# Performance work log

Hardware: AMD Instinct MI355X
Metric: run time of the kernel (lower is better)

Reference implementation:

```python
import jax, jax.numpy as jnp
import numpy as np

HID, HEADS = 2048, 16
Q_LORA, KV_LORA = 1536, 512
NOPE, ROPE, VD = 128, 64, 128
N_EXP, TOPK, MOE_I, SH_I = 8, 2, 1408, 2816
EPS, RSF = 1e-6, 1.0
ROPE_BASE = 10000.0


def _rms(x, w):
    return x * jax.lax.rsqrt(jnp.mean(jnp.square(x), -1, keepdims=True) + EPS) * w


def _rope(x, pos):
    # neox-style rotary on last dim; x: [T, H, d], pos: [T]
    d = x.shape[-1]
    inv = 1.0 / (ROPE_BASE ** (jnp.arange(0, d, 2, dtype=jnp.float32) / d))
    ang = pos.astype(jnp.float32)[:, None] * inv  # [T, d/2]
    cos, sin = jnp.cos(ang)[:, None, :], jnp.sin(ang)[:, None, :]
    x1, x2 = x[..., : d // 2], x[..., d // 2:]
    return jnp.concatenate([x1 * cos - x2 * sin, x2 * cos + x1 * sin], -1)


def setup_inputs() -> dict:
    key = jax.random.key(0)
    ks = jax.random.split(key, 16)
    T, s, f = 1024, 0.02, jnp.float32
    return {
        'positions': jnp.arange(T, dtype=jnp.int32),
        'hidden_states': jax.random.normal(ks[0], (T, HID), f),
        'residual': jax.random.normal(ks[1], (T, HID), f),
        'w_in_ln': jnp.ones((HID,), f),
        'w_post_ln': jnp.ones((HID,), f),
        'w_q_ln': jnp.ones((Q_LORA,), f),
        'w_kv_ln': jnp.ones((KV_LORA,), f),
        'w_qkv_a': jax.random.normal(ks[2], (HID, Q_LORA + KV_LORA + ROPE), f) * s,
        'w_q_b': jax.random.normal(ks[3], (Q_LORA, HEADS * (NOPE + ROPE)), f) * s,
        'w_kv_b': jax.random.normal(ks[4], (KV_LORA, HEADS * (NOPE + VD)), f) * s,
        'w_o': jax.random.normal(ks[5], (HEADS * VD, HID), f) * s,
        'gate_w': jax.random.normal(ks[6], (HID, N_EXP), f) * s,
        'we_gate': jax.random.normal(ks[7], (N_EXP, HID, MOE_I), f) * s,
        'we_up': jax.random.normal(ks[8], (N_EXP, HID, MOE_I), f) * s,
        'we_down': jax.random.normal(ks[9], (N_EXP, MOE_I, HID), f) * s,
        'ws_gate': jax.random.normal(ks[10], (HID, SH_I), f) * s,
        'ws_up': jax.random.normal(ks[11], (HID, SH_I), f) * s,
        'ws_down': jax.random.normal(ks[12], (SH_I, HID), f) * s,
    }


def reference(positions, hidden_states, residual, w_in_ln, w_post_ln, w_q_ln, w_kv_ln,
              w_qkv_a, w_q_b, w_kv_b, w_o, gate_w, we_gate, we_up, we_down,
              ws_gate, ws_up, ws_down):
    T = hidden_states.shape[0]
    # fused_add_rms_norm: residual <- x + residual; x <- rmsnorm(residual)
    residual = hidden_states + residual
    h = _rms(residual, w_in_ln)
    # fused qkv_a projection and split
    qkv = h @ w_qkv_a  # [T, q_lora + kv_lora + rope]
    q_c = _rms(qkv[:, :Q_LORA], w_q_ln)
    kv_c = _rms(qkv[:, Q_LORA:Q_LORA + KV_LORA], w_kv_ln)
    k_pe = qkv[:, Q_LORA + KV_LORA:][:, None, :]  # [T, 1, rope]
    # MLA up-projections
    q = (q_c @ w_q_b).reshape(T, HEADS, NOPE + ROPE)
    q_nope, q_pe = q[..., :NOPE], q[..., NOPE:]
    kv = (kv_c @ w_kv_b).reshape(T, HEADS, NOPE + VD)
    k_nope, v = kv[..., :NOPE], kv[..., NOPE:]
    q_pe = _rope(q_pe, positions)
    k_pe = _rope(k_pe, positions)
    q = jnp.concatenate([q_nope, q_pe], -1)  # [T, H, nope+rope]
    k = jnp.concatenate([k_nope, jnp.broadcast_to(k_pe, (T, HEADS, ROPE))], -1)
    scores = jnp.einsum('qhd,khd->hqk', q, k) * (NOPE + ROPE) ** -0.5
    causal = jnp.tril(jnp.ones((T, T), bool))
    scores = jnp.where(causal, scores, jnp.finfo(scores.dtype).min)
    p = jax.nn.softmax(scores, -1)
    attn_out = jnp.einsum('hqk,khd->qhd', p, v).reshape(T, HEADS * VD) @ w_o
    # post-attention fused add + norm
    residual = residual + attn_out
    h = _rms(residual, w_post_ln)
    # MoE gate: softmax scores, top-k, renormalized combine weights
    probs = jax.nn.softmax(h @ gate_w, -1)
    tw, ti = jax.lax.top_k(probs, TOPK)
    tw = tw / jnp.sum(tw, -1, keepdims=True)
    comb = jnp.sum(jax.nn.one_hot(ti, N_EXP, dtype=h.dtype) * tw[..., None], 1)  # [T, E]
    # routed experts (dense grouped-GEMM reference, SwiGLU)
    g = jnp.einsum('th,ehi->eti', h, we_gate)
    u = jnp.einsum('th,ehi->eti', h, we_up)
    y = jnp.einsum('eti,eih->eth', jax.nn.silu(g) * u, we_down)
    routed = jnp.einsum('te,eth->th', comb, y) * RSF
    # shared experts
    shared = (jax.nn.silu(h @ ws_gate) * (h @ ws_up)) @ ws_down
    return routed + shared, residual
```

## Files before the change

### kernel.cpp

```cpp
#include <hip/hip_runtime.h>
#include <hip/hip_bf16.h>

typedef unsigned short u16;
typedef __attribute__((ext_vector_type(8))) short bf16x8;
typedef __attribute__((ext_vector_type(4))) float f32x4;
typedef __attribute__((ext_vector_type(8))) unsigned short u16x8;
typedef __attribute__((ext_vector_type(4))) unsigned short u16x4;

#define T_TOK 1024
#define HID 2048
#define HEADS 16
#define Q_LORA 1536
#define KV_LORA 512
#define NOPE 128
#define ROPED 64
#define VD 128
#define N_EXP 8
#define MOE_I 1408
#define SH_I 2816
#define QKV_N 2112
#define QKV_LD 2176
#define QD 192
#define KVD 256
#define EPSF 1e-6f
#define NEG_BIG (-3.4e38f)

__device__ __forceinline__ u16 f2bf(float f) {
  union { float f; unsigned u; } x; x.f = f;
  unsigned r = x.u + 0x7fffu + ((x.u >> 16) & 1u);
  return (u16)(r >> 16);
}
__device__ __forceinline__ float bf2f(u16 h) {
  union { unsigned u; float f; } x; x.u = ((unsigned)h) << 16; return x.f;
}
__device__ __forceinline__ void split2(float f, u16& hi, u16& lo) {
  hi = f2bf(f);
  lo = f2bf(f - bf2f(hi));
}

__device__ __forceinline__ void gload16(const u16* g, const u16* l) {
  __builtin_amdgcn_global_load_lds(
      (const __attribute__((address_space(1))) void*)g,
      (__attribute__((address_space(3))) void*)l, 16, 0, 0);
}

__device__ __forceinline__ void xcd_unswizzle(int& bx, int& by, int& bz) {
  int gx = gridDim.x, gy = gridDim.y;
  int nwg = gx * gy * gridDim.z;
  int flat = blockIdx.x + gx * (blockIdx.y + gy * blockIdx.z);
  int q8 = nwg >> 3, r8 = nwg & 7;
  int xcd = flat & 7, pos = flat >> 3;
  int wg = (xcd < r8 ? xcd * (q8 + 1) : r8 * (q8 + 1) + (xcd - r8) * q8) + pos;
  bx = wg % gx; int tmp = wg / gx;
  by = tmp % gy; bz = tmp / gy;
}

__device__ __forceinline__ float block_sum(float v, float* s) {
  #pragma unroll
  for (int o = 32; o > 0; o >>= 1) v += __shfl_down(v, o, 64);
  int w = threadIdx.x >> 6, lane = threadIdx.x & 63;
  __syncthreads();
  if (lane == 0) s[w] = v;
  __syncthreads();
  float r = s[0];
  for (int i = 1; i < 4; ++i) r += s[i];
  return r;
}
__device__ __forceinline__ float block_max(float v, float* s) {
  #pragma unroll
  for (int o = 32; o > 0; o >>= 1) v = fmaxf(v, __shfl_down(v, o, 64));
  int w = threadIdx.x >> 6, lane = threadIdx.x & 63;
  __syncthreads();
  if (lane == 0) s[w] = v;
  __syncthreads();
  float r = s[0];
  for (int i = 1; i < 4; ++i) r = fmaxf(r, s[i]);
  return r;
}

__global__ __launch_bounds__(256) void gemm_bf16(
    const u16* __restrict__ A, long asz, int lda,
    const u16* __restrict__ B, long bsz, int ldb,
    float* __restrict__ C, u16* __restrict__ Cb, long csz, int ldc,
    const float* __restrict__ Cadd, const u16* __restrict__ CaddB, int ldcadd,
    int K, float alpha, int causal, int mode,
    float* __restrict__ pbuf, int ksplit, int stot, int soff) {
  int bxi, byi, zz;
  xcd_unswizzle(bxi, byi, zz);
  const int bm = byi << 7, bn = bxi << 7;
  const int z = (ksplit > 1) ? (zz / ksplit) : zz;
  const int s = (ksplit > 1) ? (zz % ksplit) : 0;
  A += (long)z * asz; B += (long)z * bsz;
  if (C) C += (long)z * csz;
  if (Cb) Cb += (long)z * csz;
  if (Cadd && !pbuf) Cadd += (long)z * csz;
  if (CaddB) CaddB += (long)z * csz;
  const int tid = threadIdx.x, lane = tid & 63, wid = tid >> 6;

  if (causal && bn >= bm + 128) return;

  __shared__ alignas(16) u16 As[128 * 32];
  __shared__ alignas(16) u16 Bs[128 * 32];

  const int wr = wid >> 1, wc = wid & 1;
  f32x4 acc[4][4];
  #pragma unroll
  for (int m = 0; m < 4; ++m)
    #pragma unroll
    for (int n = 0; n < 4; ++n) acc[m][n] = f32x4{0.f, 0.f, 0.f, 0.f};

  const int srow = (wid << 5) + (lane >> 2);
  const int scol = (lane & 3) << 3;
  const int arow = (wr << 6) + (lane & 15);
  const int brow = (wc << 6) + (lane & 15);
  const int koff = (lane >> 4) << 3;

  const int kseg = K / ksplit;
  const int kbeg = s * kseg, kend = kbeg + kseg;

  for (int k0 = kbeg; k0 < kend; k0 += 32) {
    #pragma unroll
    for (int c = 0; c < 2; ++c) {
      int row = srow + (c << 4);
      gload16(A + (long)(bm + row) * lda + k0 + scol, &As[(wid << 10) + (c << 9)]);
      gload16(B + (long)(bn + row) * ldb + k0 + scol, &Bs[(wid << 10) + (c << 9)]);
    }
    __syncthreads();
    bf16x8 a[4], b[4];
    #pragma unroll
    for (int m = 0; m < 4; ++m) a[m] = *(const bf16x8*)&As[((arow + (m << 4)) << 5) + koff];
    #pragma unroll
    for (int n = 0; n < 4; ++n) b[n] = *(const bf16x8*)&Bs[((brow + (n << 4)) << 5) + koff];
    #pragma unroll
    for (int m = 0; m < 4; ++m)
      #pragma unroll
      for (int n = 0; n < 4; ++n)
        acc[m][n] = __builtin_amdgcn_mfma_f32_16x16x32_bf16(a[m], b[n], acc[m][n], 0, 0, 0);
    __syncthreads();
  }

  const int rbase = bm + (wr << 6) + ((lane >> 4) << 2);
  const int cbase = bn + (wc << 6) + (lane & 15);

  if (pbuf) {
    long pstride = (long)(gridDim.y << 7) * ldc;
    float* pp = pbuf + ((long)z * stot + soff + s) * pstride;
    #pragma unroll
    for (int m = 0; m < 4; ++m)
      #pragma unroll
      for (int j = 0; j < 4; ++j) {
        int r = rbase + (m << 4) + j;
        #pragma unroll
        for (int n = 0; n < 4; ++n) {
          int cc = cbase + (n << 4);
          pp[(long)r * ldc + cc] = acc[m][n][j];
        }
      }
    return;
  }

  #pragma unroll
  for (int m = 0; m < 4; ++m) {
    #pragma unroll
    for (int j = 0; j < 4; ++j) {
      int r = rbase + (m << 4) + j;
      #pragma unroll
      for (int n = 0; n < 4; ++n) {
        int cc = cbase + (n << 4);
        float v = acc[m][n][j] * alpha;
        if (mode == 0) {
          if (Cadd) v += Cadd[(long)r * ldcadd + cc];
          if (causal && cc > r) v = NEG_BIG;
          C[(long)r * ldc + cc] = v;
        } else if (mode == 1) {
          float gg = Cadd[(long)r * ldcadd + cc];
          float sgv = gg / (1.f + expf(-gg));
          Cb[(long)r * ldc + cc] = f2bf(sgv * v);
        } else if (mode == 2) {
          Cb[(long)r * ldc + cc] = f2bf(v);
        } else {
          float gg = bf2f(CaddB[(long)r * ldcadd + cc]);
          float sgv = gg / (1.f + expf(-gg));
          Cb[(long)r * ldc + cc] = f2bf(sgv * v);
        }
      }
    }
  }
}

__global__ __launch_bounds__(256) void reduce_sk(
    const float* __restrict__ pbuf, long pstride, int S,
    float* __restrict__ C, u16* __restrict__ Cb, long csz, int ldc, int Nc,
    const float* __restrict__ Cadd, long caddsz, int ldcadd,
    float alpha, int mode) {
  const int z = blockIdx.y;
  const float* pz = pbuf + (long)z * S * pstride;
  long idx = ((long)blockIdx.x * 256 + threadIdx.x) * 8;
  long r = idx / Nc; int c = (int)(idx - r * Nc);
  float a[8] = {0.f, 0.f, 0.f, 0.f, 0.f, 0.f, 0.f, 0.f};
  for (int s = 0; s < S; ++s) {
    const float* pp = pz + (long)s * pstride + idx;
    float4 x = *(const float4*)pp;
    float4 y = *(const float4*)(pp + 4);
    a[0] += x.x; a[1] += x.y; a[2] += x.z; a[3] += x.w;
    a[4] += y.x; a[5] += y.y; a[6] += y.z; a[7] += y.w;
  }
  long ob = (long)z * csz + r * ldc + c;
  if (mode == 0) {
    #pragma unroll
    for (int k = 0; k < 8; ++k) {
      float v = a[k] * alpha;
      if (Cadd) v += Cadd[(long)z * caddsz + r * ldcadd + c + k];
      C[ob + k] = v;
    }
  } else {
    u16x8 o;
    #pragma unroll
    for (int k = 0; k < 8; ++k) {
      float gg = Cadd[(long)z * caddsz + r * ldcadd + c + k];
      float sgv = gg / (1.f + expf(-gg));
      o[k] = f2bf(sgv * a[k] * alpha);
    }
    *(u16x8*)&Cb[ob] = o;
  }
}

__global__ __launch_bounds__(256) void transpose_f32_bf16(
    const float* __restrict__ src, long sbs, int ld_src, int Cvalid,
    u16* __restrict__ dst, long dbs, int ld_dst) {
  __shared__ float tile[64][65];
  src += (long)blockIdx.z * sbs; dst += (long)blockIdx.z * dbs;
  const int c0 = blockIdx.x << 6, r0 = blockIdx.y << 6;
  const int tid = threadIdx.x;
  const int tc = (tid & 15) << 2, tr0 = tid >> 4;
  const bool valid = c0 < Cvalid;
  #pragma unroll
  for (int i = 0; i < 4; ++i) {
    int r = tr0 + (i << 4);
    float4 v;
    if (valid) v = *(const float4*)&src[(long)(r0 + r) * ld_src + c0 + tc];
    else { v.x = 0.f; v.y = 0.f; v.z = 0.f; v.w = 0.f; }
    tile[r][tc] = v.x; tile[r][tc + 1] = v.y; tile[r][tc + 2] = v.z; tile[r][tc + 3] = v.w;
  }
  __syncthreads();
  const int oc = tid >> 2, seg = tid & 3;
  u16x8 o0, o1;
  #pragma unroll
  for (int k = 0; k < 8; ++k) o0[k] = f2bf(tile[(seg << 4) + k][oc]);
  #pragma unroll
  for (int k = 0; k < 8; ++k) o1[k] = f2bf(tile[(seg << 4) + 8 + k][oc]);
  u16* dp = &dst[(long)(c0 + oc) * ld_dst + r0 + (seg << 4)];
  *(u16x8*)dp = o0;
  *(u16x8*)(dp + 8) = o1;
}

__global__ __launch_bounds__(256) void transpose_split3(
    const float* __restrict__ src, long sbs, int ld_src, int Cvalid,
    u16* __restrict__ dst, long dbs, int Kp) {
  __shared__ float tile[64][65];
  src += (long)blockIdx.z * sbs; dst += (long)blockIdx.z * dbs;
  const int c0 = blockIdx.x << 6, r0 = blockIdx.y << 6;
  const int tid = threadIdx.x;
  const int tc = (tid & 15) << 2, tr0 = tid >> 4;
  const bool valid = c0 < Cvalid;
  #pragma unroll
  for (int i = 0; i < 4; ++i) {
    int r = tr0 + (i << 4);
    float4 v;
    if (valid) v = *(const float4*)&src[(long)(r0 + r) * ld_src + c0 + tc];
    else { v.x = 0.f; v.y = 0.f; v.z = 0.f; v.w = 0.f; }
    tile[r][tc] = v.x; tile[r][tc + 1] = v.y; tile[r][tc + 2] = v.z; tile[r][tc + 3] = v.w;
  }
  __syncthreads();
  const int oc = tid >> 2, seg = tid & 3;
  u16x8 h0, h1, l0, l1;
  #pragma unroll
  for (int k = 0; k < 8; ++k) {
    u16 hi, lo; split2(tile[(seg << 4) + k][oc], hi, lo);
    h0[k] = hi; l0[k] = lo;
  }
  #pragma unroll
  for (int k = 0; k < 8; ++k) {
    u16 hi, lo; split2(tile[(seg << 4) + 8 + k][oc], hi, lo);
    h1[k] = hi; l1[k] = lo;
  }
  const int ldd = 3 * Kp;
  u16* dp = &dst[(long)(c0 + oc) * ldd + r0 + (seg << 4)];
  *(u16x8*)dp = h0;            *(u16x8*)(dp + 8) = h1;
  *(u16x8*)(dp + Kp) = h0;     *(u16x8*)(dp + Kp + 8) = h1;
  *(u16x8*)(dp + 2 * Kp) = l0; *(u16x8*)(dp + 2 * Kp + 8) = l1;
}

__global__ __launch_bounds__(256) void conv_split3_kernel(
    const float* __restrict__ src, u16* __restrict__ dst, int C, long n) {
  long stride = (long)gridDim.x * 2048;
  for (long i = ((long)blockIdx.x * 256 + threadIdx.x) * 8; i < n; i += stride) {
    long r = i / C; int c = (int)(i - r * C);
    float4 a = *(const float4*)&src[i];
    float4 b = *(const float4*)&src[i + 4];
    u16x8 hv, lv;
    u16 hi, lo;
    split2(a.x, hi, lo); hv[0] = hi; lv[0] = lo;
    split2(a.y, hi, lo); hv[1] = hi; lv[1] = lo;
    split2(a.z, hi, lo); hv[2] = hi; lv[2] = lo;
    split2(a.w, hi, lo); hv[3] = hi; lv[3] = lo;
    split2(b.x, hi, lo); hv[4] = hi; lv[4] = lo;
    split2(b.y, hi, lo); hv[5] = hi; lv[5] = lo;
    split2(b.z, hi, lo); hv[6] = hi; lv[6] = lo;
    split2(b.w, hi, lo); hv[7] = hi; lv[7] = lo;
    u16* base = dst + r * (long)(3 * C) + c;
    *(u16x8*)base = hv;
    *(u16x8*)(base + C) = lv;
    *(u16x8*)(base + 2 * C) = hv;
  }
}

__global__ __launch_bounds__(256) void add_rms_kernel(
    const float* __restrict__ hs, const float* __restrict__ res,
    const float* __restrict__ w, float* __restrict__ resid1, u16* __restrict__ h3) {
  __shared__ float sbuf[4];
  int t = blockIdx.x;
  float v[8]; float ss = 0.f;
  #pragma unroll
  for (int i = 0; i < 8; ++i) {
    int j = threadIdx.x + (i << 8);
    float x = hs[(long)t * HID + j] + res[(long)t * HID + j];
    v[i] = x; resid1[(long)t * HID + j] = x; ss += x * x;
  }
  ss = block_sum(ss, sbuf);
  float sc = rsqrtf(ss / (float)HID + EPSF);
  u16* base = h3 + (long)t * (3 * HID);
  #pragma unroll
  for (int i = 0; i < 8; ++i) {
    int j = threadIdx.x + (i << 8);
    u16 hi, lo; split2(v[i] * sc * w[j], hi, lo);
    base[j] = hi; base[HID + j] = lo; base[2 * HID + j] = hi;
  }
}

template <int NW, bool SPLIT, bool WF32>
__global__ __launch_bounds__(256) void rms_rows_kernel(
    const float* __restrict__ in, int ldin, const float* __restrict__ w,
    u16* __restrict__ outb, float* __restrict__ outf) {
  __shared__ float sbuf[4];
  int t = blockIdx.x;
  const int W = NW * 256;
  float v[NW]; float ss = 0.f;
  #pragma unroll
  for (int i = 0; i < NW; ++i) {
    int j = threadIdx.x + (i << 8);
    float x = in[(long)t * ldin + j];
    v[i] = x; ss += x * x;
  }
  ss = block_sum(ss, sbuf);
  float sc = rsqrtf(ss / (float)W + EPSF);
  #pragma unroll
  for (int i = 0; i < NW; ++i) {
    int j = threadIdx.x + (i << 8);
    float y = v[i] * sc * w[j];
    if (SPLIT) {
      u16 hi, lo; split2(y, hi, lo);
      u16* base = outb + (long)t * (3 * W);
      base[j] = hi; base[W + j] = lo; base[2 * W + j] = hi;
    } else {
      outb[(long)t * W + j] = f2bf(y);
    }
    if (WF32) outf[(long)t * W + j] = y;
  }
}

__global__ __launch_bounds__(256) void rope_kernel(
    const int* __restrict__ pos, float* __restrict__ q,
    const float* __restrict__ qkv, float* __restrict__ kpe) {
  int t = blockIdx.x;
  float fp = (float)pos[t];
  for (int item = threadIdx.x; item < 544; item += 256) {
    int i = item & 31;
    float inv = expf(-((float)i * (2.f / 64.f)) * 9.210340371976184f);
    float ang = fp * inv;
    float c = cosf(ang), s = sinf(ang);
    if (item < 512) {
      int hh = item >> 5;
      long base = (long)t * (HEADS * QD) + hh * QD + NOPE;
      float x1 = q[base + i], x2 = q[base + 32 + i];
      q[base + i] = x1 * c - x2 * s;
      q[base + 32 + i] = x2 * c + x1 * s;
    } else {
      long base = (long)t * QKV_LD + (Q_LORA + KV_LORA);
      float x1 = qkv[base + i], x2 = qkv[base + 32 + i];
      kpe[(long)t * 64 + i] = x1 * c - x2 * s;
      kpe[(long)t * 64 + 32 + i] = x2 * c + x1 * s;
    }
  }
}

__global__ __launch_bounds__(192) void build_q3_kernel(
    const float* __restrict__ qbuf, u16* __restrict__ q3) {
  int t = blockIdx.x, h = blockIdx.y, d = threadIdx.x;
  float x = qbuf[(long)t * (HEADS * QD) + h * QD + d];
  u16 hi, lo; split2(x, hi, lo);
  u16* base = q3 + ((long)h * T_TOK + t) * (3 * QD);
  base[d] = hi; base[QD + d] = lo; base[2 * QD + d] = hi;
}

__global__ __launch_bounds__(192) void build_kmat3_kernel(
    const float* __restrict__ kv, const float* __restrict__ kpe,
    u16* __restrict__ kmat3) {
  int t = blockIdx.x, h = blockIdx.y, d = threadIdx.x;
  float v = (d < NOPE) ? kv[(long)t * (HEADS * KVD) + h * KVD + d]
                       : kpe[(long)t * 64 + (d - NOPE)];
  u16 hi, lo; split2(v, hi, lo);
  u16* base = kmat3 + ((long)h * T_TOK + t) * (3 * QD);
  base[d] = hi; base[QD + d] = hi; base[2 * QD + d] = lo;
}

__global__ __launch_bounds__(256) void softmax_kernel(
    const float* __restrict__ S, u16* __restrict__ P2) {
  __shared__ float sbuf[4];
  long row = blockIdx.x;
  int r = (int)(row & (T_TOK - 1));
  const float* p = S + row * T_TOK;
  float4 v = ((const float4*)p)[threadIdx.x];
  int c0 = threadIdx.x << 2;
  if (c0 + 0 > r) v.x = NEG_BIG;
  if (c0 + 1 > r) v.y = NEG_BIG;
  if (c0 + 2 > r) v.z = NEG_BIG;
  if (c0 + 3 > r) v.w = NEG_BIG;
  float m = fmaxf(fmaxf(v.x, v.y), fmaxf(v.z, v.w));
  m = block_max(m, sbuf);
  v.x = expf(v.x - m); v.y = expf(v.y - m); v.z = expf(v.z - m); v.w = expf(v.w - m);
  float s = v.x + v.y + v.z + v.w;
  s = block_sum(s, sbuf);
  float inv = 1.f / s;
  u16x4 hv, lv;
  u16 hi, lo;
  split2(v.x * inv, hi, lo); hv[0] = hi; lv[0] = lo;
  split2(v.y * inv, hi, lo); hv[1] = hi; lv[1] = lo;
  split2(v.z * inv, hi, lo); hv[2] = hi; lv[2] = lo;
  split2(v.w * inv, hi, lo); hv[3] = hi; lv[3] = lo;
  u16* base = P2 + row * (2 * T_TOK) + (threadIdx.x << 2);
  *(u16x4*)base = hv;
  *(u16x4*)(base + T_TOK) = lv;
}

__global__ __launch_bounds__(256) void gate_topk_kernel(
    const float* __restrict__ h2, const float* __restrict__ gw,
    float* __restrict__ comb) {
  __shared__ float sbuf[4];
  __shared__ float lg[N_EXP];
  int t = blockIdx.x;
  float p[N_EXP] = {0.f, 0.f, 0.f, 0.f, 0.f, 0.f, 0.f, 0.f};
  for (int j = threadIdx.x; j < HID; j += 256) {
    float x = h2[(long)t * HID + j];
    const float* gr = gw + (long)j * N_EXP;
    #pragma unroll
    for (int e = 0; e < N_EXP; ++e) p[e] += x * gr[e];
  }
  #pragma unroll
  for (int e = 0; e < N_EXP; ++e) {
    float s = block_sum(p[e], sbuf);
    if (threadIdx.x == 0) lg[e] = s;
  }
  __syncthreads();
  if (threadIdx.x == 0) {
    float m = lg[0];
    for (int e = 1; e < N_EXP; ++e) m = fmaxf(m, lg[e]);
    float pe[N_EXP]; float s = 0.f;
    for (int e = 0; e < N_EXP; ++e) { pe[e] = expf(lg[e] - m); s += pe[e]; }
    for (int e = 0; e < N_EXP; ++e) pe[e] /= s;
    int i0 = 0;
    for (int e = 1; e < N_EXP; ++e) if (pe[e] > pe[i0]) i0 = e;
    int i1 = -1;
    for (int e = 0; e < N_EXP; ++e) if (e != i0 && (i1 < 0 || pe[e] > pe[i1])) i1 = e;
    float ssum = pe[i0] + pe[i1];
    for (int e = 0; e < N_EXP; ++e) comb[(long)t * N_EXP + e] = 0.f;
    comb[(long)t * N_EXP + i0] = pe[i0] / ssum;
    comb[(long)t * N_EXP + i1] = pe[i1] / ssum;
  }
}

__global__ __launch_bounds__(256) void combine_out_kernel(
    const u16* __restrict__ y, const float* __restrict__ comb,
    float* __restrict__ out0) {
  int t = blockIdx.x;
  int j = threadIdx.x << 3;
  float a[8] = {0.f, 0.f, 0.f, 0.f, 0.f, 0.f, 0.f, 0.f};
  for (int e = 0; e < N_EXP; ++e) {
    float ce = comb[(long)t * N_EXP + e];
    if (ce == 0.f) continue;
    u16x8 v = *(const u16x8*)&y[((long)e * T_TOK + t) * HID + j];
    #pragma unroll
    for (int k = 0; k < 8; ++k) a[k] += ce * bf2f(v[k]);
  }
  #pragma unroll
  for (int e = 8; e < 10; ++e) {
    u16x8 v = *(const u16x8*)&y[((long)e * T_TOK + t) * HID + j];
    #pragma unroll
    for (int k = 0; k < 8; ++k) a[k] += bf2f(v[k]);
  }
  float* rp = out0 + (long)t * HID + j;
  #pragma unroll
  for (int k = 0; k < 8; ++k) rp[k] = a[k];
}

extern "C" void kernel_launch(void* const* d_in, const int* in_sizes, int n_in,
                              void* d_out, int out_size, void* d_ws, size_t ws_size,
                              hipStream_t stream) {
  (void)in_sizes; (void)n_in; (void)out_size; (void)ws_size;
  const int*   positions = (const int*)d_in[0];
  const float* hs        = (const float*)d_in[1];
  const float* res       = (const float*)d_in[2];
  const float* w_in_ln   = (const float*)d_in[3];
  const float* w_post_ln = (const float*)d_in[4];
  const float* w_q_ln    = (const float*)d_in[5];
  const float* w_kv_ln   = (const float*)d_in[6];
  const float* w_qkv_a   = (const float*)d_in[7];
  const float* w_q_b     = (const float*)d_in[8];
  const float* w_kv_b    = (const float*)d_in[9];
  const float* w_o       = (const float*)d_in[10];
  const float* gate_w    = (const float*)d_in[11];
  const float* we_gate   = (const float*)d_in[12];
  const float* we_up     = (const float*)d_in[13];
  const float* we_down   = (const float*)d_in[14];
  const float* ws_gate   = (const float*)d_in[15];
  const float* ws_up     = (const float*)d_in[16];
  const float* ws_dn     = (const float*)d_in[17];

  float* out0   = (float*)d_out;
  float* resid2 = out0 + (long)T_TOK * HID;

  char* Wb = (char*)d_ws;
  size_t off = 0;
  #define CARVE(name, type, bytes) type* name = (type*)(Wb + off); off += (((size_t)(bytes) + 255) & ~(size_t)255)

  CARVE(wqkvaT3, u16, (size_t)QKV_LD * 3 * HID * 2);
  CARVE(wqbT3,   u16, (size_t)(HEADS * QD) * 3 * Q_LORA * 2);
  CARVE(wkvbT3,  u16, (size_t)(HEADS * KVD) * 3 * KV_LORA * 2);
  CARVE(woT3,    u16, (size_t)HID * 3 * HID * 2);

  size_t pool = off;
  CARVE(resid1, float, (size_t)T_TOK * HID * 4);
  CARVE(h3,     u16,   (size_t)T_TOK * 3 * HID * 2);
  CARVE(qkv,    float, (size_t)T_TOK * QKV_LD * 4);
  CARVE(qc3,    u16,   (size_t)T_TOK * 3 * Q_LORA * 2);
  CARVE(kvc3,   u16,   (size_t)T_TOK * 3 * KV_LORA * 2);
  CARVE(qbuf,   float, (size_t)T_TOK * HEADS * QD * 4);
  CARVE(q3,     u16,   (size_t)HEADS * T_TOK * 3 * QD * 2);
  CARVE(kvbuf,  float, (size_t)T_TOK * HEADS * KVD * 4);
  CARVE(kpe,    float, (size_t)T_TOK * 64 * 4);
  CARVE(kmat3,  u16,   (size_t)HEADS * T_TOK * 3 * QD * 2);
  CARVE(vt3,    u16,   (size_t)HEADS * VD * 3 * T_TOK * 2);
  CARVE(scores, float, (size_t)HEADS * T_TOK * T_TOK * 4);
  CARVE(P2,     u16,   (size_t)HEADS * T_TOK * 2 * T_TOK * 2);
  CARVE(attn,   float, (size_t)T_TOK * HID * 4);
  CARVE(attn3,  u16,   (size_t)T_TOK * 3 * HID * 2);
  size_t endA = off;
  float* pbufA = scores;

  off = pool;
  CARVE(wegT10, u16, (size_t)10 * MOE_I * HID * 2);
  CARVE(weuT10, u16, (size_t)10 * MOE_I * HID * 2);
  CARVE(wedT10, u16, (size_t)10 * HID * MOE_I * 2);
  CARVE(h2,     float, (size_t)T_TOK * HID * 4);
  CARVE(h2_b,   u16,   (size_t)T_TOK * HID * 2);
  CARVE(comb,   float, (size_t)T_TOK * N_EXP * 4);
  CARVE(gact_g, u16,   (size_t)10 * T_TOK * MOE_I * 2);
  CARVE(gact,   u16,   (size_t)10 * T_TOK * MOE_I * 2);
  CARVE(ybuf16, u16,   (size_t)10 * T_TOK * HID * 2);
  if (off < endA) off = endA;
  #undef CARVE

  const float* nullf = nullptr;
  float* nullC = nullptr;
  u16* nullB = nullptr;
  const u16* nullBB = nullptr;

  hipLaunchKernelGGL(transpose_split3, dim3(QKV_LD / 64, HID / 64, 1), dim3(256), 0, stream,
                     w_qkv_a, 0L, QKV_N, QKV_N, wqkvaT3, 0L, HID);
  hipLaunchKernelGGL(transpose_split3, dim3(HEADS * QD / 64, Q_LORA / 64, 1), dim3(256), 0, stream,
                     w_q_b, 0L, HEADS * QD, HEADS * QD, wqbT3, 0L, Q_LORA);
  hipLaunchKernelGGL(transpose_split3, dim3(HEADS * KVD / 64, KV_LORA / 64, 1), dim3(256), 0, stream,
                     w_kv_b, 0L, HEADS * KVD, HEADS * KVD, wkvbT3, 0L, KV_LORA);
  hipLaunchKernelGGL(transpose_split3, dim3(HID / 64, HID / 64, 1), dim3(256), 0, stream,
                     w_o, 0L, HID, HID, woT3, 0L, HID);

  hipLaunchKernelGGL(add_rms_kernel, dim3(T_TOK), dim3(256), 0, stream,
                     hs, res, w_in_ln, resid1, h3);
  hipLaunchKernelGGL(gemm_bf16, dim3(QKV_LD / 128, T_TOK / 128, 4), dim3(256), 0, stream,
                     h3, 0L, 3 * HID, wqkvaT3, 0L, 3 * HID,
                     nullC, nullB, 0L, QKV_LD, nullf, nullBB, 0, 3 * HID, 1.f, 0, 0,
                     pbufA, 4, 4, 0);
  hipLaunchKernelGGL(reduce_sk, dim3(T_TOK * QKV_LD / 2048, 1), dim3(256), 0, stream,
                     pbufA, (long)T_TOK * QKV_LD, 4,
                     qkv, nullB, 0L, QKV_LD, QKV_LD, nullf, 0L, 0, 1.f, 0);
  hipLaunchKernelGGL((rms_rows_kernel<6, true, false>), dim3(T_TOK), dim3(256), 0, stream,
                     qkv, QKV_LD, w_q_ln, qc3, (float*)nullptr);
  hipLaunchKernelGGL((rms_rows_kernel<2, true, false>), dim3(T_TOK), dim3(256), 0, stream,
                     qkv + Q_LORA, QKV_LD, w_kv_ln, kvc3, (float*)nullptr);
  hipLaunchKernelGGL(gemm_bf16, dim3(HEADS * QD / 128, T_TOK / 128, 4), dim3(256), 0, stream,
                     qc3, 0L, 3 * Q_LORA, wqbT3, 0L, 3 * Q_LORA,
                     nullC, nullB, 0L, HEADS * QD, nullf, nullBB, 0, 3 * Q_LORA, 1.f, 0, 0,
                     pbufA, 4, 4, 0);
  hipLaunchKernelGGL(reduce_sk, dim3(T_TOK * HEADS * QD / 2048, 1), dim3(256), 0, stream,
                     pbufA, (long)T_TOK * HEADS * QD, 4,
                     qbuf, nullB, 0L, HEADS * QD, HEADS * QD, nullf, 0L, 0, 1.f, 0);
  hipLaunchKernelGGL(gemm_bf16, dim3(HEADS * KVD / 128, T_TOK / 128, 4), dim3(256), 0, stream,
                     kvc3, 0L, 3 * KV_LORA, wkvbT3, 0L, 3 * KV_LORA,
                     nullC, nullB, 0L, HEADS * KVD, nullf, nullBB, 0, 3 * KV_LORA, 1.f, 0, 0,
                     pbufA, 4, 4, 0);
  hipLaunchKernelGGL(reduce_sk, dim3(T_TOK * HEADS * KVD / 2048, 1), dim3(256), 0, stream,
                     pbufA, (long)T_TOK * HEADS * KVD, 4,
                     kvbuf, nullB, 0L, HEADS * KVD, HEADS * KVD, nullf, 0L, 0, 1.f, 0);
  hipLaunchKernelGGL(rope_kernel, dim3(T_TOK), dim3(256), 0, stream,
                     positions, qbuf, qkv, kpe);
  hipLaunchKernelGGL(build_q3_kernel, dim3(T_TOK, HEADS), dim3(192), 0, stream, qbuf, q3);
  hipLaunchKernelGGL(build_kmat3_kernel, dim3(T_TOK, HEADS), dim3(192), 0, stream,
                     kvbuf, kpe, kmat3);
  hipLaunchKernelGGL(transpose_split3, dim3(VD / 64, T_TOK / 64, HEADS), dim3(256), 0, stream,
                     kvbuf + NOPE, 256L, HEADS * KVD, VD, vt3, (long)VD * 3 * T_TOK, T_TOK);
  hipLaunchKernelGGL(gemm_bf16, dim3(T_TOK / 128, T_TOK / 128, HEADS), dim3(256), 0, stream,
                     q3, (long)T_TOK * 3 * QD, 3 * QD,
                     kmat3, (long)T_TOK * 3 * QD, 3 * QD,
                     scores, nullB, (long)T_TOK * T_TOK, T_TOK,
                     nullf, nullBB, 0, 576, 0.07216878364870322f, 1, 0,
                     nullC, 1, 1, 0);
  hipLaunchKernelGGL(softmax_kernel, dim3(HEADS * T_TOK), dim3(256), 0, stream, scores, P2);
  hipLaunchKernelGGL(gemm_bf16, dim3(VD / 128, T_TOK / 128, HEADS * 4), dim3(256), 0, stream,
                     P2, (long)T_TOK * 2 * T_TOK, 2 * T_TOK,
                     vt3, (long)VD * 3 * T_TOK, 3 * T_TOK,
                     nullC, nullB, 0L, VD, nullf, nullBB, 0, 2 * T_TOK, 1.f, 0, 0,
                     pbufA, 4, 6, 0);
  hipLaunchKernelGGL(gemm_bf16, dim3(VD / 128, T_TOK / 128, HEADS * 2), dim3(256), 0, stream,
                     P2, (long)T_TOK * 2 * T_TOK, 2 * T_TOK,
                     vt3 + 2 * T_TOK, (long)VD * 3 * T_TOK, 3 * T_TOK,
                     nullC, nullB, 0L, VD, nullf, nullBB, 0, T_TOK, 1.f, 0, 0,
                     pbufA, 2, 6, 4);
  hipLaunchKernelGGL(reduce_sk, dim3(T_TOK * VD / 2048, HEADS), dim3(256), 0, stream,
                     pbufA, (long)T_TOK * VD, 6,
                     attn, nullB, (long)VD, HID, VD, nullf, 0L, 0, 1.f, 0);
  hipLaunchKernelGGL(conv_split3_kernel, dim3(1024), dim3(256), 0, stream,
                     attn, attn3, HID, (long)T_TOK * HID);
  hipLaunchKernelGGL(gemm_bf16, dim3(HID / 128, T_TOK / 128, 4), dim3(256), 0, stream,
                     attn3, 0L, 3 * HID, woT3, 0L, 3 * HID,
                     nullC, nullB, 0L, HID, nullf, nullBB, 0, 3 * HID, 1.f, 0, 0,
                     pbufA, 4, 4, 0);
  hipLaunchKernelGGL(reduce_sk, dim3(T_TOK * HID / 2048, 1), dim3(256), 0, stream,
                     pbufA, (long)T_TOK * HID, 4,
                     resid2, nullB, 0L, HID, HID, resid1, 0L, HID, 1.f, 0);

  hipLaunchKernelGGL(transpose_f32_bf16, dim3(MOE_I / 64, HID / 64, N_EXP), dim3(256), 0, stream,
                     we_gate, (long)HID * MOE_I, MOE_I, MOE_I, wegT10, (long)MOE_I * HID, HID);
  hipLaunchKernelGGL(transpose_f32_bf16, dim3(MOE_I / 64, HID / 64, 2), dim3(256), 0, stream,
                     ws_gate, (long)MOE_I, SH_I, MOE_I,
                     wegT10 + (size_t)8 * MOE_I * HID, (long)MOE_I * HID, HID);
  hipLaunchKernelGGL(transpose_f32_bf16, dim3(MOE_I / 64, HID / 64, N_EXP), dim3(256), 0, stream,
                     we_up, (long)HID * MOE_I, MOE_I, MOE_I, weuT10, (long)MOE_I * HID, HID);
  hipLaunchKernelGGL(transpose_f32_bf16, dim3(MOE_I / 64, HID / 64, 2), dim3(256), 0, stream,
                     ws_up, (long)MOE_I, SH_I, MOE_I,
                     weuT10 + (size_t)8 * MOE_I * HID, (long)MOE_I * HID, HID);
  hipLaunchKernelGGL(transpose_f32_bf16, dim3(HID / 64, MOE_I / 64, N_EXP), dim3(256), 0, stream,
                     we_down, (long)MOE_I * HID, HID, HID, wedT10, (long)HID * MOE_I, MOE_I);
  hipLaunchKernelGGL(transpose_f32_bf16, dim3(HID / 64, MOE_I / 64, 2), dim3(256), 0, stream,
                     ws_dn, (long)MOE_I * HID, HID, HID,
                     wedT10 + (size_t)8 * HID * MOE_I, (long)HID * MOE_I, MOE_I);

  hipLaunchKernelGGL((rms_rows_kernel<8, false, true>), dim3(T_TOK), dim3(256), 0, stream,
                     resid2, HID, w_post_ln, h2_b, h2);
  hipLaunchKernelGGL(gate_topk_kernel, dim3(T_TOK), dim3(256), 0, stream,
                     h2, gate_w, comb);
  hipLaunchKernelGGL(gemm_bf16, dim3(MOE_I / 128, T_TOK / 128, 10), dim3(256), 0, stream,
                     h2_b, 0L, HID, wegT10, (long)MOE_I * HID, HID,
                     nullC, gact_g, (long)T_TOK * MOE_I, MOE_I,
                     nullf, nullBB, 0, HID, 1.f, 0, 2, nullC, 1, 1, 0);
  hipLaunchKernelGGL(gemm_bf16, dim3(MOE_I / 128, T_TOK / 128, 10), dim3(256), 0, stream,
                     h2_b, 0L, HID, weuT10, (long)MOE_I * HID, HID,
                     nullC, gact, (long)T_TOK * MOE_I, MOE_I,
                     nullf, gact_g, MOE_I, HID, 1.f, 0, 3, nullC, 1, 1, 0);
  hipLaunchKernelGGL(gemm_bf16, dim3(HID / 128, T_TOK / 128, 10), dim3(256), 0, stream,
                     gact, (long)T_TOK * MOE_I, MOE_I,
                     wedT10, (long)HID * MOE_I, MOE_I,
                     nullC, ybuf16, (long)T_TOK * HID, HID,
                     nullf, nullBB, 0, MOE_I, 1.f, 0, 2, nullC, 1, 1, 0);
  hipLaunchKernelGGL(combine_out_kernel, dim3(T_TOK), dim3(256), 0, stream,
                     ybuf16, comb, out0);
}
```

Before: 984.1 us.

## Route MoE tokens via gathered index lists instead of dense all-expert GEMMs

Replaces dense evaluation of every expert on all tokens with a sparse grouped GEMM. A routing kernel builds per-expert token lists, and the GEMMs gather A rows by index and skip row tiles beyond each expert's count. This removes about three quarters of the routed-expert FLOPs. The combine step now reads only the two selected expert outputs plus the shared ones. The XCD block unswizzle is also dropped, which may hurt L2 locality across the other GEMMs.

```diff
diff --git a/kernel.cpp b/kernel.cpp
--- a/kernel.cpp
+++ b/kernel.cpp
@@ -44,17 +44,6 @@
       (__attribute__((address_space(3))) void*)l, 16, 0, 0);
 }
 
-__device__ __forceinline__ void xcd_unswizzle(int& bx, int& by, int& bz) {
-  int gx = gridDim.x, gy = gridDim.y;
-  int nwg = gx * gy * gridDim.z;
-  int flat = blockIdx.x + gx * (blockIdx.y + gy * blockIdx.z);
-  int q8 = nwg >> 3, r8 = nwg & 7;
-  int xcd = flat & 7, pos = flat >> 3;
-  int wg = (xcd < r8 ? xcd * (q8 + 1) : r8 * (q8 + 1) + (xcd - r8) * q8) + pos;
-  bx = wg % gx; int tmp = wg / gx;
-  by = tmp % gy; bz = tmp / gy;
-}
-
 __device__ __forceinline__ float block_sum(float v, float* s) {
   #pragma unroll
   for (int o = 32; o > 0; o >>= 1) v += __shfl_down(v, o, 64);
@@ -84,12 +73,13 @@
     float* __restrict__ C, u16* __restrict__ Cb, long csz, int ldc,
     const float* __restrict__ Cadd, const u16* __restrict__ CaddB, int ldcadd,
     int K, float alpha, int causal, int mode,
-    float* __restrict__ pbuf, int ksplit, int stot, int soff) {
-  int bxi, byi, zz;
-  xcd_unswizzle(bxi, byi, zz);
-  const int bm = byi << 7, bn = bxi << 7;
+    float* __restrict__ pbuf, int ksplit, int stot, int soff,
+    const int* __restrict__ gidx, const int* __restrict__ gcnt) {
+  const int bm = blockIdx.y << 7, bn = blockIdx.x << 7;
+  const int zz = blockIdx.z;
   const int z = (ksplit > 1) ? (zz / ksplit) : zz;
   const int s = (ksplit > 1) ? (zz % ksplit) : 0;
+  if (gcnt && bm >= gcnt[z]) return;
   A += (long)z * asz; B += (long)z * bsz;
   if (C) C += (long)z * csz;
   if (Cb) Cb += (long)z * csz;
@@ -115,16 +105,25 @@
   const int brow = (wc << 6) + (lane & 15);
   const int koff = (lane >> 4) << 3;
 
+  long ga0, ga1;
+  {
+    int r0 = srow, r1 = srow + 16;
+    if (gidx) {
+      const int* tk = gidx + (long)z * T_TOK;
+      ga0 = (long)tk[bm + r0]; ga1 = (long)tk[bm + r1];
+    } else {
+      ga0 = (long)(bm + r0); ga1 = (long)(bm + r1);
+    }
+  }
+
   const int kseg = K / ksplit;
   const int kbeg = s * kseg, kend = kbeg + kseg;
 
   for (int k0 = kbeg; k0 < kend; k0 += 32) {
-    #pragma unroll
-    for (int c = 0; c < 2; ++c) {
-      int row = srow + (c << 4);
-      gload16(A + (long)(bm + row) * lda + k0 + scol, &As[(wid << 10) + (c << 9)]);
-      gload16(B + (long)(bn + row) * ldb + k0 + scol, &Bs[(wid << 10) + (c << 9)]);
-    }
+    gload16(A + ga0 * lda + k0 + scol, &As[(wid << 10)]);
+    gload16(A + ga1 * lda + k0 + scol, &As[(wid << 10) + 512]);
+    gload16(B + (long)(bn + srow) * ldb + k0 + scol, &Bs[(wid << 10)]);
+    gload16(B + (long)(bn + srow + 16) * ldb + k0 + scol, &Bs[(wid << 10) + 512]);
     __syncthreads();
     bf16x8 a[4], b[4];
     #pragma unroll
@@ -445,7 +444,7 @@
 
 __global__ __launch_bounds__(256) void gate_topk_kernel(
     const float* __restrict__ h2, const float* __restrict__ gw,
-    float* __restrict__ comb) {
+    int* __restrict__ ti, float* __restrict__ tw) {
   __shared__ float sbuf[4];
   __shared__ float lg[N_EXP];
   int t = blockIdx.x;
@@ -473,34 +472,56 @@
     int i1 = -1;
     for (int e = 0; e < N_EXP; ++e) if (e != i0 && (i1 < 0 || pe[e] > pe[i1])) i1 = e;
     float ssum = pe[i0] + pe[i1];
-    for (int e = 0; e < N_EXP; ++e) comb[(long)t * N_EXP + e] = 0.f;
-    comb[(long)t * N_EXP + i0] = pe[i0] / ssum;
-    comb[(long)t * N_EXP + i1] = pe[i1] / ssum;
-  }
+    ti[2 * t] = i0; ti[2 * t + 1] = i1;
+    tw[2 * t] = pe[i0] / ssum; tw[2 * t + 1] = pe[i1] / ssum;
+  }
+}
+
+__global__ __launch_bounds__(64) void route_build_kernel(
+    const int* __restrict__ ti, int* __restrict__ tokidx,
+    int* __restrict__ pos, int* __restrict__ cnt) {
+  int e = blockIdx.x;
+  int lane = threadIdx.x;
+  if (e >= N_EXP) {
+    for (int p = lane; p < T_TOK; p += 64) tokidx[(long)e * T_TOK + p] = p;
+    if (lane == 0) cnt[e] = T_TOK;
+    return;
+  }
+  int c = 0;
+  for (int base = 0; base < T_TOK; base += 64) {
+    int t = base + lane;
+    int e0 = ti[2 * t], e1 = ti[2 * t + 1];
+    bool match = (e0 == e) || (e1 == e);
+    unsigned long long mask = __ballot(match);
+    int pref = __popcll(mask & ((1ull << lane) - 1ull));
+    if (match) {
+      int p = c + pref;
+      tokidx[(long)e * T_TOK + p] = t;
+      pos[2 * t + ((e0 == e) ? 0 : 1)] = p;
+    }
+    c += __popcll(mask);
+  }
+  for (int p = c + lane; p < T_TOK; p += 64) tokidx[(long)e * T_TOK + p] = 0;
+  if (lane == 0) cnt[e] = c;
 }
 
 __global__ __launch_bounds__(256) void combine_out_kernel(
-    const u16* __restrict__ y, const float* __restrict__ comb,
+    const u16* __restrict__ y, const int* __restrict__ ti,
+    const float* __restrict__ tw, const int* __restrict__ pos,
     float* __restrict__ out0) {
   int t = blockIdx.x;
   int j = threadIdx.x << 3;
-  float a[8] = {0.f, 0.f, 0.f, 0.f, 0.f, 0.f, 0.f, 0.f};
-  for (int e = 0; e < N_EXP; ++e) {
-    float ce = comb[(long)t * N_EXP + e];
-    if (ce == 0.f) continue;
-    u16x8 v = *(const u16x8*)&y[((long)e * T_TOK + t) * HID + j];
-    #pragma unroll
-    for (int k = 0; k < 8; ++k) a[k] += ce * bf2f(v[k]);
-  }
-  #pragma unroll
-  for (int e = 8; e < 10; ++e) {
-    u16x8 v = *(const u16x8*)&y[((long)e * T_TOK + t) * HID + j];
-    #pragma unroll
-    for (int k = 0; k < 8; ++k) a[k] += bf2f(v[k]);
-  }
+  int e0 = ti[2 * t], e1 = ti[2 * t + 1];
+  int p0 = pos[2 * t], p1 = pos[2 * t + 1];
+  float w0 = tw[2 * t], w1 = tw[2 * t + 1];
+  u16x8 a = *(const u16x8*)&y[((long)e0 * T_TOK + p0) * HID + j];
+  u16x8 b = *(const u16x8*)&y[((long)e1 * T_TOK + p1) * HID + j];
+  u16x8 c = *(const u16x8*)&y[((long)8 * T_TOK + t) * HID + j];
+  u16x8 d = *(const u16x8*)&y[((long)9 * T_TOK + t) * HID + j];
   float* rp = out0 + (long)t * HID + j;
   #pragma unroll
-  for (int k = 0; k < 8; ++k) rp[k] = a[k];
+  for (int k = 0; k < 8; ++k)
+    rp[k] = w0 * bf2f(a[k]) + w1 * bf2f(b[k]) + bf2f(c[k]) + bf2f(d[k]);
 }
 
 extern "C" void kernel_launch(void* const* d_in, const int* in_sizes, int n_in,
@@ -563,10 +584,14 @@
   CARVE(wedT10, u16, (size_t)10 * HID * MOE_I * 2);
   CARVE(h2,     float, (size_t)T_TOK * HID * 4);
   CARVE(h2_b,   u16,   (size_t)T_TOK * HID * 2);
-  CARVE(comb,   float, (size_t)T_TOK * N_EXP * 4);
+  CARVE(ti,     int,   (size_t)T_TOK * 2 * 4);
+  CARVE(tw,     float, (size_t)T_TOK * 2 * 4);
+  CARVE(pos,    int,   (size_t)T_TOK * 2 * 4);
+  CARVE(tokidx, int,   (size_t)10 * T_TOK * 4);
+  CARVE(cnt,    int,   64);
   CARVE(gact_g, u16,   (size_t)10 * T_TOK * MOE_I * 2);
   CARVE(gact,   u16,   (size_t)10 * T_TOK * MOE_I * 2);
-  CARVE(ybuf16, u16,   (size_t)10 * T_TOK * HID * 2);
+  CARVE(ycomp,  u16,   (size_t)10 * T_TOK * HID * 2);
   if (off < endA) off = endA;
   #undef CARVE
 
@@ -574,6 +599,7 @@
   float* nullC = nullptr;
   u16* nullB = nullptr;
   const u16* nullBB = nullptr;
+  const int* nullI = nullptr;
 
   hipLaunchKernelGGL(transpose_split3, dim3(QKV_LD / 64, HID / 64, 1), dim3(256), 0, stream,
                      w_qkv_a, 0L, QKV_N, QKV_N, wqkvaT3, 0L, HID);
@@ -589,7 +615,7 @@
   hipLaunchKernelGGL(gemm_bf16, dim3(QKV_LD / 128, T_TOK / 128, 4), dim3(256), 0, stream,
                      h3, 0L, 3 * HID, wqkvaT3, 0L, 3 * HID,
                      nullC, nullB, 0L, QKV_LD, nullf, nullBB, 0, 3 * HID, 1.f, 0, 0,
-                     pbufA, 4, 4, 0);
+                     pbufA, 4, 4, 0, nullI, nullI);
   hipLaunchKernelGGL(reduce_sk, dim3(T_TOK * QKV_LD / 2048, 1), dim3(256), 0, stream,
                      pbufA, (long)T_TOK * QKV_LD, 4,
                      qkv, nullB, 0L, QKV_LD, QKV_LD, nullf, 0L, 0, 1.f, 0);
@@ -600,14 +626,14 @@
   hipLaunchKernelGGL(gemm_bf16, dim3(HEADS * QD / 128, T_TOK / 128, 4), dim3(256), 0, stream,
                      qc3, 0L, 3 * Q_LORA, wqbT3, 0L, 3 * Q_LORA,
                      nullC, nullB, 0L, HEADS * QD, nullf, nullBB, 0, 3 * Q_LORA, 1.f, 0, 0,
-                     pbufA, 4, 4, 0);
+                     pbufA, 4, 4, 0, nullI, nullI);
   hipLaunchKernelGGL(reduce_sk, dim3(T_TOK * HEADS * QD / 2048, 1), dim3(256), 0, stream,
                      pbufA, (long)T_TOK * HEADS * QD, 4,
                      qbuf, nullB, 0L, HEADS * QD, HEADS * QD, nullf, 0L, 0, 1.f, 0);
   hipLaunchKernelGGL(gemm_bf16, dim3(HEADS * KVD / 128, T_TOK / 128, 4), dim3(256), 0, stream,
                      kvc3, 0L, 3 * KV_LORA, wkvbT3, 0L, 3 * KV_LORA,
                      nullC, nullB, 0L, HEADS * KVD, nullf, nullBB, 0, 3 * KV_LORA, 1.f, 0, 0,
-                     pbufA, 4, 4, 0);
+                     pbufA, 4, 4, 0, nullI, nullI);
   hipLaunchKernelGGL(reduce_sk, dim3(T_TOK * HEADS * KVD / 2048, 1), dim3(256), 0, stream,
                      pbufA, (long)T_TOK * HEADS * KVD, 4,
                      kvbuf, nullB, 0L, HEADS * KVD, HEADS * KVD, nullf, 0L, 0, 1.f, 0);
@@ -623,18 +649,18 @@
                      kmat3, (long)T_TOK * 3 * QD, 3 * QD,
                      scores, nullB, (long)T_TOK * T_TOK, T_TOK,
                      nullf, nullBB, 0, 576, 0.07216878364870322f, 1, 0,
-                     nullC, 1, 1, 0);
+                     nullC, 1, 1, 0, nullI, nullI);
   hipLaunchKernelGGL(softmax_kernel, dim3(HEADS * T_TOK), dim3(256), 0, stream, scores, P2);
   hipLaunchKernelGGL(gemm_bf16, dim3(VD / 128, T_TOK / 128, HEADS * 4), dim3(256), 0, stream,
                      P2, (long)T_TOK * 2 * T_TOK, 2 * T_TOK,
                      vt3, (long)VD * 3 * T_TOK, 3 * T_TOK,
                      nullC, nullB, 0L, VD, nullf, nullBB, 0, 2 * T_TOK, 1.f, 0, 0,
-                     pbufA, 4, 6, 0);
+                     pbufA, 4, 6, 0, nullI, nullI);
   hipLaunchKernelGGL(gemm_bf16, dim3(VD / 128, T_TOK / 128, HEADS * 2), dim3(256), 0, stream,
                      P2, (long)T_TOK * 2 * T_TOK, 2 * T_TOK,
                      vt3 + 2 * T_TOK, (long)VD * 3 * T_TOK, 3 * T_TOK,
                      nullC, nullB, 0L, VD, nullf, nullBB, 0, T_TOK, 1.f, 0, 0,
-                     pbufA, 2, 6, 4);
+                     pbufA, 2, 6, 4, nullI, nullI);
   hipLaunchKernelGGL(reduce_sk, dim3(T_TOK * VD / 2048, HEADS), dim3(256), 0, stream,
                      pbufA, (long)T_TOK * VD, 6,
                      attn, nullB, (long)VD, HID, VD, nullf, 0L, 0, 1.f, 0);
@@ -643,7 +669,7 @@
   hipLaunchKernelGGL(gemm_bf16, dim3(HID / 128, T_TOK / 128, 4), dim3(256), 0, stream,
                      attn3, 0L, 3 * HID, woT3, 0L, 3 * HID,
                      nullC, nullB, 0L, HID, nullf, nullBB, 0, 3 * HID, 1.f, 0, 0,
-                     pbufA, 4, 4, 0);
+                     pbufA, 4, 4, 0, nullI, nullI);
   hipLaunchKernelGGL(reduce_sk, dim3(T_TOK * HID / 2048, 1), dim3(256), 0, stream,
                      pbufA, (long)T_TOK * HID, 4,
                      resid2, nullB, 0L, HID, HID, resid1, 0L, HID, 1.f, 0);
@@ -667,20 +693,22 @@
   hipLaunchKernelGGL((rms_rows_kernel<8, false, true>), dim3(T_TOK), dim3(256), 0, stream,
                      resid2, HID, w_post_ln, h2_b, h2);
   hipLaunchKernelGGL(gate_topk_kernel, dim3(T_TOK), dim3(256), 0, stream,
-                     h2, gate_w, comb);
+                     h2, gate_w, ti, tw);
+  hipLaunchKernelGGL(route_build_kernel, dim3(10), dim3(64), 0, stream,
+                     ti, tokidx, pos, cnt);
   hipLaunchKernelGGL(gemm_bf16, dim3(MOE_I / 128, T_TOK / 128, 10), dim3(256), 0, stream,
                      h2_b, 0L, HID, wegT10, (long)MOE_I * HID, HID,
                      nullC, gact_g, (long)T_TOK * MOE_I, MOE_I,
-                     nullf, nullBB, 0, HID, 1.f, 0, 2, nullC, 1, 1, 0);
+                     nullf, nullBB, 0, HID, 1.f, 0, 2, nullC, 1, 1, 0, tokidx, cnt);
   hipLaunchKernelGGL(gemm_bf16, dim3(MOE_I / 128, T_TOK / 128, 10), dim3(256), 0, stream,
                      h2_b, 0L, HID, weuT10, (long)MOE_I * HID, HID,
                      nullC, gact, (long)T_TOK * MOE_I, MOE_I,
-                     nullf, gact_g, MOE_I, HID, 1.f, 0, 3, nullC, 1, 1, 0);
+                     nullf, gact_g, MOE_I, HID, 1.f, 0, 3, nullC, 1, 1, 0, tokidx, cnt);
   hipLaunchKernelGGL(gemm_bf16, dim3(HID / 128, T_TOK / 128, 10), dim3(256), 0, stream,
                      gact, (long)T_TOK * MOE_I, MOE_I,
                      wedT10, (long)HID * MOE_I, MOE_I,
-                     nullC, ybuf16, (long)T_TOK * HID, HID,
-                     nullf, nullBB, 0, MOE_I, 1.f, 0, 2, nullC, 1, 1, 0);
+                     nullC, ycomp, (long)T_TOK * HID, HID,
+                     nullf, nullBB, 0, MOE_I, 1.f, 0, 2, nullC, 1, 1, 0, nullI, cnt);
   hipLaunchKernelGGL(combine_out_kernel, dim3(T_TOK), dim3(256), 0, stream,
-                     ybuf16, comb, out0);
-}
+                     ycomp, ti, tw, pos, out0);
+}
```

New measurement: 914.3 us. -7.1%, faster.
